# Optimization experiments

Measured on AMD Instinct MI355X. Metric: run time of the kernel, lower is better.

Reference implementation:

```python
import jax, jax.numpy as jnp
import numpy as np
from jax import lax


def _conv1d(x, w, b, stride, pad):
    # x: [N, 1, L], w: [1, 1, K]
    y = lax.conv_general_dilated(x, w, (stride,), [(pad, pad)],
                                 dimension_numbers=('NCH', 'OIH', 'NCH'))
    return y + b[None, :, None]


def _maxpool1d(x, k, stride, pad):
    # torch MaxPool1d semantics: pad with -inf, window max
    return lax.reduce_window(x, -jnp.inf, lax.max,
                             (1, 1, k), (1, 1, stride),
                             ((0, 0), (0, 0), (pad, pad)))


def setup_inputs() -> dict:
    key = jax.random.key(0)
    ks = jax.random.split(key, 14)
    bs, n, T = 64, 1024, 1200
    return {
        'input':   jax.random.normal(ks[0], (bs, n, T), jnp.float32),
        'conv1_w': jax.random.normal(ks[1], (1, 1, 10), jnp.float32) * 0.3,
        'conv1_b': jax.random.normal(ks[2], (1,), jnp.float32) * 0.1,
        'conv2_w': jax.random.normal(ks[3], (1, 1, 3), jnp.float32) * 0.5,
        'conv2_b': jax.random.normal(ks[4], (1,), jnp.float32) * 0.1,
        'conv3_w': jax.random.normal(ks[5], (1, 1, 4), jnp.float32) * 0.5,
        'conv3_b': jax.random.normal(ks[6], (1,), jnp.float32) * 0.1,
        'gcn1_w':  jax.random.normal(ks[7], (30, 30), jnp.float32) * 0.18,
        'gcn1_b':  jax.random.normal(ks[8], (30,), jnp.float32) * 0.1,
        'gcn2_w':  jax.random.normal(ks[9], (4, 4), jnp.float32) * 0.5,
        'gcn2_b':  jax.random.normal(ks[10], (4,), jnp.float32) * 0.1,
        'cls_w':   jax.random.normal(ks[11], (3, n), jnp.float32) * 0.03,
        'cls_b':   jax.random.normal(ks[12], (3,), jnp.float32) * 0.1,
    }


def reference(input, conv1_w, conv1_b, conv2_w, conv2_b, conv3_w, conv3_b,
              gcn1_w, gcn1_b, gcn2_w, gcn2_b, cls_w, cls_b):
    bs, n, T = input.shape
    # Per-node 1-channel conv chain: fold nodes into the batch dim (replaces
    # the original Python loop over num_nodes issuing tiny Conv1d launches).
    x = input.reshape(bs * n, 1, T)
    h = jax.nn.relu(_conv1d(x, conv1_w, conv1_b, 8, 1))   # L: 1200 -> 150
    h = jax.nn.relu(_maxpool1d(h, 5, 5, 0))               # 150 -> 30
    # NOTE: original applies gcn1 to t_layer_out[2] here, but overwrites an
    # already-consumed list entry -> output is DEAD w.r.t. the final result.
    # (GCNConv over the all-ones adjacency == mean over nodes @ W.T + b.)
    h = jax.nn.relu(_conv1d(h, conv2_w, conv2_b, 3, 0))   # 30 -> 10
    h = jax.nn.relu(_maxpool1d(h, 3, 3, 1))               # 10 -> 4
    # Same dead-code situation for gcn2 on t_layer_out[4].
    h = jax.nn.relu(_conv1d(h, conv3_w, conv3_b, 1, 0))   # 4 -> 1
    feat = h.reshape(bs, n)                               # L5 == 1
    logits = feat @ cls_w.T + cls_b
    return jax.nn.softmax(logits, axis=1)
```

## Files before the change

kernel.cpp:

```cpp
#include <hip/hip_runtime.h>


#define T_LEN 1200
#define NROWS (64 * 1024)

__global__ __launch_bounds__(256) void row_chain_kernel(
    const float* __restrict__ input,
    const float* __restrict__ w1, const float* __restrict__ b1,
    const float* __restrict__ w2, const float* __restrict__ b2,
    const float* __restrict__ w3, const float* __restrict__ b3,
    float* __restrict__ feat)
{
    __shared__ __align__(16) float xs[T_LEN];
    __shared__ float y1[152];
    __shared__ float p1[32];
    __shared__ float y2[10];

    const int tid = threadIdx.x;
    const size_t row = blockIdx.x;

    const float4* src = (const float4*)(input + row * T_LEN);
    float4* dst = (float4*)xs;
    for (int i = tid; i < T_LEN / 4; i += 256) {
        dst[i] = src[i];
    }
    __syncthreads();

    if (tid < 150) {
        float acc = b1[0];
        const int base = tid * 8 - 1;
        #pragma unroll
        for (int k = 0; k < 10; ++k) {
            const int idx = base + k;
            const float v = (idx >= 0 && idx < T_LEN) ? xs[idx] : 0.0f;
            acc = fmaf(w1[k], v, acc);
        }
        y1[tid] = fmaxf(acc, 0.0f);
    }
    __syncthreads();

    if (tid < 30) {
        float m = y1[tid * 5];
        #pragma unroll
        for (int k = 1; k < 5; ++k) m = fmaxf(m, y1[tid * 5 + k]);
        p1[tid] = m;
    }
    __syncthreads();

    if (tid < 10) {
        float acc = b2[0];
        #pragma unroll
        for (int k = 0; k < 3; ++k) acc = fmaf(w2[k], p1[tid * 3 + k], acc);
        y2[tid] = fmaxf(acc, 0.0f);
    }
    __syncthreads();

    if (tid == 0) {
        const float q0 = fmaxf(y2[0], y2[1]);
        const float q1 = fmaxf(fmaxf(y2[2], y2[3]), y2[4]);
        const float q2 = fmaxf(fmaxf(y2[5], y2[6]), y2[7]);
        const float q3 = fmaxf(y2[8], y2[9]);
        float f = b3[0];
        f = fmaf(w3[0], q0, f);
        f = fmaf(w3[1], q1, f);
        f = fmaf(w3[2], q2, f);
        f = fmaf(w3[3], q3, f);
        feat[row] = fmaxf(f, 0.0f);
    }
}

__global__ __launch_bounds__(256) void classifier_kernel(
    const float* __restrict__ feat,
    const float* __restrict__ cls_w,
    const float* __restrict__ cls_b,
    float* __restrict__ out)
{
    const int b = blockIdx.x;
    const int tid = threadIdx.x;

    float s0 = 0.0f, s1 = 0.0f, s2 = 0.0f;
    for (int n = tid; n < 1024; n += 256) {
        const float f = feat[b * 1024 + n];
        s0 = fmaf(f, cls_w[n], s0);
        s1 = fmaf(f, cls_w[1024 + n], s1);
        s2 = fmaf(f, cls_w[2048 + n], s2);
    }
    #pragma unroll
    for (int off = 32; off > 0; off >>= 1) {
        s0 += __shfl_down(s0, off, 64);
        s1 += __shfl_down(s1, off, 64);
        s2 += __shfl_down(s2, off, 64);
    }
    __shared__ float red[3][4];
    const int wave = tid >> 6;
    if ((tid & 63) == 0) {
        red[0][wave] = s0;
        red[1][wave] = s1;
        red[2][wave] = s2;
    }
    __syncthreads();
    if (tid == 0) {
        const float l0 = red[0][0] + red[0][1] + red[0][2] + red[0][3] + cls_b[0];
        const float l1 = red[1][0] + red[1][1] + red[1][2] + red[1][3] + cls_b[1];
        const float l2 = red[2][0] + red[2][1] + red[2][2] + red[2][3] + cls_b[2];
        const float m = fmaxf(l0, fmaxf(l1, l2));
        const float e0 = expf(l0 - m);
        const float e1 = expf(l1 - m);
        const float e2 = expf(l2 - m);
        const float inv = 1.0f / (e0 + e1 + e2);
        out[b * 3 + 0] = e0 * inv;
        out[b * 3 + 1] = e1 * inv;
        out[b * 3 + 2] = e2 * inv;
    }
}

extern "C" void kernel_launch(void* const* d_in, const int* in_sizes, int n_in,
                              void* d_out, int out_size, void* d_ws, size_t ws_size,
                              hipStream_t stream) {
    const float* input   = (const float*)d_in[0];
    const float* conv1_w = (const float*)d_in[1];
    const float* conv1_b = (const float*)d_in[2];
    const float* conv2_w = (const float*)d_in[3];
    const float* conv2_b = (const float*)d_in[4];
    const float* conv3_w = (const float*)d_in[5];
    const float* conv3_b = (const float*)d_in[6];
    const float* cls_w   = (const float*)d_in[11];
    const float* cls_b   = (const float*)d_in[12];

    float* feat = (float*)d_ws;
    float* out  = (float*)d_out;

    row_chain_kernel<<<NROWS, 256, 0, stream>>>(
        input, conv1_w, conv1_b, conv2_w, conv2_b, conv3_w, conv3_b, feat);
    classifier_kernel<<<64, 256, 0, stream>>>(feat, cls_w, cls_b, out);
}
```

Before: 425.1 us.

## Stream conv1 and pool1 per thread in registers and split out the tail stage

The one-block-per-row kernel, which staged each row in shared memory and synced four times, is replaced by a kernel where each thread handles a third of a row. The thread streams 40-float chunks through registers with float4 loads and fuses conv1, ReLU and the max pool, carrying boundary values between chunks. The pooled results go to workspace, and a separate per-row kernel computes conv2, pool2 and conv3. This removes mostly idle threads, shared-memory staging and barriers. In exchange, each thread's loads are strided by 1600 bytes across the wave, which hurts coalescing, and an extra kernel launch and workspace round trip are added.

```diff
diff --git a/kernel.cpp b/kernel.cpp
--- a/kernel.cpp
+++ b/kernel.cpp
@@ -1,72 +1,97 @@
 #include <hip/hip_runtime.h>
 
 
-#define T_LEN 1200
-#define NROWS (64 * 1024)
+#define NROWS 65536
+#define P1_STRIDE 32
 
-__global__ __launch_bounds__(256) void row_chain_kernel(
+__global__ __launch_bounds__(256, 3) void conv1_pool1_kernel(
     const float* __restrict__ input,
-    const float* __restrict__ w1, const float* __restrict__ b1,
-    const float* __restrict__ w2, const float* __restrict__ b2,
-    const float* __restrict__ w3, const float* __restrict__ b3,
+    const float* __restrict__ w1g, const float* __restrict__ b1g,
+    float* __restrict__ p1out)
+{
+    const int t = blockIdx.x * 256 + threadIdx.x;
+    const int row = t / 3;
+    const int s = t - row * 3;
+    const float* rowp = input + (size_t)row * 1200 + s * 400;
+    const float4* rp4 = (const float4*)rowp;
+
+    float w1[10];
+    #pragma unroll
+    for (int k = 0; k < 10; ++k) w1[k] = w1g[k];
+    const float b1 = b1g[0];
+
+    float carry = (s == 0) ? 0.0f : rowp[-1];
+
+    float4 cur[10], nxt[10];
+    #pragma unroll
+    for (int q = 0; q < 10; ++q) cur[q] = rp4[q];
+
+    float* out = p1out + (size_t)row * P1_STRIDE + s * 10;
+
+    #pragma unroll 1
+    for (int w = 0; w < 10; ++w) {
+        float la;
+        if (w < 9) {
+            #pragma unroll
+            for (int q = 0; q < 10; ++q) nxt[q] = rp4[(w + 1) * 10 + q];
+            la = nxt[0].x;
+        } else {
+            la = (s < 2) ? rowp[400] : 0.0f;
+        }
+
+        const float* f = (const float*)cur;
+        float pmax = 0.0f;
+        #pragma unroll
+        for (int i = 0; i < 5; ++i) {
+            const float x_m1 = (i == 0) ? carry : f[8 * i - 1];
+            const float x_p8 = (i == 4) ? la : f[8 * i + 8];
+            float acc = b1;
+            acc = fmaf(w1[0], x_m1, acc);
+            #pragma unroll
+            for (int k = 1; k <= 8; ++k) acc = fmaf(w1[k], f[8 * i - 1 + k], acc);
+            acc = fmaf(w1[9], x_p8, acc);
+            pmax = fmaxf(pmax, acc);
+        }
+        out[w] = pmax;
+
+        carry = f[39];
+        #pragma unroll
+        for (int q = 0; q < 10; ++q) cur[q] = nxt[q];
+    }
+}
+
+__global__ __launch_bounds__(256) void tail_kernel(
+    const float* __restrict__ p1,
+    const float* __restrict__ w2g, const float* __restrict__ b2g,
+    const float* __restrict__ w3g, const float* __restrict__ b3g,
     float* __restrict__ feat)
 {
-    __shared__ __align__(16) float xs[T_LEN];
-    __shared__ float y1[152];
-    __shared__ float p1[32];
-    __shared__ float y2[10];
+    const int row = blockIdx.x * 256 + threadIdx.x;
+    const float* p = p1 + (size_t)row * P1_STRIDE;
 
-    const int tid = threadIdx.x;
-    const size_t row = blockIdx.x;
+    const float w2a = w2g[0], w2b = w2g[1], w2c = w2g[2];
+    const float b2 = b2g[0];
 
-    const float4* src = (const float4*)(input + row * T_LEN);
-    float4* dst = (float4*)xs;
-    for (int i = tid; i < T_LEN / 4; i += 256) {
-        dst[i] = src[i];
+    float y2[10];
+    #pragma unroll
+    for (int j = 0; j < 10; ++j) {
+        float acc = b2;
+        acc = fmaf(w2a, p[3 * j], acc);
+        acc = fmaf(w2b, p[3 * j + 1], acc);
+        acc = fmaf(w2c, p[3 * j + 2], acc);
+        y2[j] = fmaxf(acc, 0.0f);
     }
-    __syncthreads();
+    const float q0 = fmaxf(y2[0], y2[1]);
+    const float q1 = fmaxf(fmaxf(y2[2], y2[3]), y2[4]);
+    const float q2 = fmaxf(fmaxf(y2[5], y2[6]), y2[7]);
+    const float q3 = fmaxf(y2[8], y2[9]);
 
-    if (tid < 150) {
-        float acc = b1[0];
-        const int base = tid * 8 - 1;
-        #pragma unroll
-        for (int k = 0; k < 10; ++k) {
-            const int idx = base + k;
-            const float v = (idx >= 0 && idx < T_LEN) ? xs[idx] : 0.0f;
-            acc = fmaf(w1[k], v, acc);
-        }
-        y1[tid] = fmaxf(acc, 0.0f);
-    }
-    __syncthreads();
-
-    if (tid < 30) {
-        float m = y1[tid * 5];
-        #pragma unroll
-        for (int k = 1; k < 5; ++k) m = fmaxf(m, y1[tid * 5 + k]);
-        p1[tid] = m;
-    }
-    __syncthreads();
-
-    if (tid < 10) {
-        float acc = b2[0];
-        #pragma unroll
-        for (int k = 0; k < 3; ++k) acc = fmaf(w2[k], p1[tid * 3 + k], acc);
-        y2[tid] = fmaxf(acc, 0.0f);
-    }
-    __syncthreads();
-
-    if (tid == 0) {
-        const float q0 = fmaxf(y2[0], y2[1]);
-        const float q1 = fmaxf(fmaxf(y2[2], y2[3]), y2[4]);
-        const float q2 = fmaxf(fmaxf(y2[5], y2[6]), y2[7]);
-        const float q3 = fmaxf(y2[8], y2[9]);
-        float f = b3[0];
-        f = fmaf(w3[0], q0, f);
-        f = fmaf(w3[1], q1, f);
-        f = fmaf(w3[2], q2, f);
-        f = fmaf(w3[3], q3, f);
-        feat[row] = fmaxf(f, 0.0f);
-    }
+    float f = b3g[0];
+    f = fmaf(w3g[0], q0, f);
+    f = fmaf(w3g[1], q1, f);
+    f = fmaf(w3g[2], q2, f);
+    f = fmaf(w3g[3], q3, f);
+    feat[row] = fmaxf(f, 0.0f);
 }
 
 __global__ __launch_bounds__(256) void classifier_kernel(
@@ -127,10 +152,14 @@
     const float* cls_w   = (const float*)d_in[11];
     const float* cls_b   = (const float*)d_in[12];
 
-    float* feat = (float*)d_ws;
+    float* wsf  = (float*)d_ws;
+    float* feat = wsf;
+    float* p1   = wsf + NROWS;
     float* out  = (float*)d_out;
 
-    row_chain_kernel<<<NROWS, 256, 0, stream>>>(
-        input, conv1_w, conv1_b, conv2_w, conv2_b, conv3_w, conv3_b, feat);
+    conv1_pool1_kernel<<<(NROWS * 3) / 256, 256, 0, stream>>>(
+        input, conv1_w, conv1_b, p1);
+    tail_kernel<<<NROWS / 256, 256, 0, stream>>>(
+        p1, conv2_w, conv2_b, conv3_w, conv3_b, feat);
     classifier_kernel<<<64, 256, 0, stream>>>(feat, cls_w, cls_b, out);
 }
```

New measurement: 463.7 us. +9.1%, slower.
